# Performance work log

Hardware: AMD Instinct MI355X
Metric: run time of the kernel (lower is better)

## Reference

```python
import jax, jax.numpy as jnp
import numpy as np

B, S, M, D, H, NH = 8, 1024, 2048, 512, 512, 8  # batch, seq, mem slots, memory_dim, hidden_dim, heads
THRESHOLD = 0.5
DECAY = 0.95


def setup_inputs() -> dict:
    key = jax.random.key(0)
    ks = jax.random.split(key, 16)
    def w(k, shape, s=0.02):
        return jax.random.normal(k, shape, jnp.float32) * s
    z = lambda n: jnp.zeros((n,), jnp.float32)
    return {
        'new_info': jax.random.normal(ks[0], (B, S, D), jnp.float32),
        'memory_bank': jax.random.normal(ks[1], (B, M, D), jnp.float32),
        'W_in': w(ks[2], (D, H)), 'b_in': z(H),
        'Wq': w(ks[3], (H, H)), 'bq': z(H),
        'Wk': w(ks[4], (H, H)), 'bk': z(H),
        'Wv': w(ks[5], (H, H)), 'bv': z(H),
        'Wo': w(ks[6], (H, H)), 'bo': z(H),
        'Wi1': w(ks[7], (H, H // 2)), 'bi1': z(H // 2),
        'Wi2': w(ks[8], (H // 2, 1)), 'bi2': z(1),
        'Wu1': w(ks[9], (2 * H, H)), 'bu1': z(H),
        'Wu2': w(ks[10], (H, H)), 'bu2': z(H),
    }


def _mha(q, k, v, Wq, bq, Wk, bk, Wv, bv, Wo, bo):
    # torch nn.MultiheadAttention math (batch_first, eval mode / no dropout)
    b, mq, h = q.shape
    d = h // NH
    qh = (q @ Wq + bq).reshape(b, mq, NH, d)
    kh = (k @ Wk + bk).reshape(b, -1, NH, d)
    vh = (v @ Wv + bv).reshape(b, -1, NH, d)
    scores = jnp.einsum('bqhd,bkhd->bhqk', qh, kh) / np.float32(np.sqrt(d))
    attn = jax.nn.softmax(scores, axis=-1)
    out = jnp.einsum('bhqk,bkhd->bqhd', attn, vh).reshape(b, mq, h)
    return out @ Wo + bo


def reference(new_info, memory_bank, W_in, b_in, Wq, bq, Wk, bk, Wv, bv, Wo, bo,
              Wi1, bi1, Wi2, bi2, Wu1, bu1, Wu2, bu2):
    # project new info + memory into hidden space
    info_proj = new_info @ W_in + b_in                       # [B,S,H]
    mem_proj = memory_bank @ W_in + b_in                     # [B,M,H]
    # per-token importance (sigmoid MLP)
    imp = jax.nn.sigmoid(jax.nn.relu(info_proj @ Wi1 + bi1) @ Wi2 + bi2)[..., 0]  # [B,S]
    # cross-attention: memory slots attend to new tokens -> per-slot write weights
    attn_out = _mha(mem_proj, info_proj, info_proj, Wq, bq, Wk, bk, Wv, bv, Wo, bo)  # [B,M,H]
    # scale write weights by importance (vectorized reading of the original broadcast)
    write_weights = attn_out * jnp.mean(imp, axis=1)[:, None, None]  # [B,M,H]
    # write-position selection: argmax over memory slots (importance scalar is positive,
    # so in the original all qualifying tokens of a batch pick the same slot)
    pos = jnp.argmax(jnp.mean(write_weights, axis=-1), axis=1)      # [B]
    mask = imp > THRESHOLD                                          # [B,S]
    exists = jnp.any(mask, axis=1)                                  # [B]
    # original loop overwrites the slot for each qualifying s, always reading the
    # ORIGINAL memory_bank -> final value comes from the LAST qualifying token
    s_star = S - 1 - jnp.argmax(mask[:, ::-1], axis=1)              # [B]
    bidx = jnp.arange(B)
    sel = new_info[bidx, s_star]                                    # [B,D]
    old = memory_bank[bidx, pos]                                    # [B,D]
    comb = jnp.concatenate([old, sel], axis=-1)                     # [B,2D]
    upd = jnp.tanh(jax.nn.relu(comb @ Wu1 + bu1) @ Wu2 + bu2)       # [B,H]
    ww = write_weights[bidx, pos]                                   # [B,H]
    new_mem = jnp.where(exists[:, None], old + upd * ww, old)
    updated = memory_bank.at[bidx, pos].set(new_mem)
    # forgetting: memory_age defaults to zeros -> decay_rate**0 == 1 (kept for fidelity)
    decay = jnp.power(jnp.float32(DECAY), jnp.zeros((M,), jnp.float32))
    updated = updated * decay[None, :, None]
    return updated, write_weights, imp
```

## Files before the change

kernel.cpp:

```cpp
#include <hip/hip_runtime.h>
#include <hip/hip_bf16.h>
#include <math.h>

#define BB 8
#define SS 1024
#define MM 2048
#define DD 512
#define HH 512
#define NHEAD 8
#define DHEAD 64

typedef __attribute__((ext_vector_type(8))) short short8;
typedef __attribute__((ext_vector_type(4))) float f32x4;
typedef unsigned short us;

__device__ __forceinline__ us bf_hi(float x) {
    __hip_bfloat16 h = __float2bfloat16(x);
    return *reinterpret_cast<const us*>(&h);
}
__device__ __forceinline__ float bf_f(us h) {
    return __uint_as_float(((unsigned)h) << 16);
}
__device__ __forceinline__ void split_pack4(float a, float b, float c, float d,
                                            uint2& hp, uint2& lp) {
    us h0 = bf_hi(a), h1 = bf_hi(b), h2 = bf_hi(c), h3 = bf_hi(d);
    hp.x = (unsigned)h0 | ((unsigned)h1 << 16);
    hp.y = (unsigned)h2 | ((unsigned)h3 << 16);
    us l0 = bf_hi(a - bf_f(h0)), l1 = bf_hi(b - bf_f(h1));
    us l2 = bf_hi(c - bf_f(h2)), l3 = bf_hi(d - bf_f(h3));
    lp.x = (unsigned)l0 | ((unsigned)l1 << 16);
    lp.y = (unsigned)l2 | ((unsigned)l3 << 16);
}
__device__ __forceinline__ uint2 pack4_hi(float a, float b, float c, float d) {
    uint2 hp;
    hp.x = (unsigned)bf_hi(a) | ((unsigned)bf_hi(b) << 16);
    hp.y = (unsigned)bf_hi(c) | ((unsigned)bf_hi(d) << 16);
    return hp;
}

__device__ __forceinline__ void gload_lds16(const void* g, void* l) {
    __builtin_amdgcn_global_load_lds(
        (__attribute__((address_space(1))) void*)(g),
        (__attribute__((address_space(3))) void*)(l), 16, 0, 0);
}

struct TSB {
    const float* src[6];
    us* dh[6];
    us* dl[6];
    int nc[6];
};

__global__ __launch_bounds__(256) void prep_all(
    const float* __restrict__ x, float* __restrict__ cpy,
    us* __restrict__ hi, us* __restrict__ lo, int n8, float* __restrict__ zbuf,
    const float* __restrict__ bk, const float* __restrict__ bv,
    float* __restrict__ bkv,
    const float* __restrict__ b_in, const float* __restrict__ Wq,
    const float* __restrict__ bq, float* __restrict__ bq_eff, TSB a)
{
    __shared__ float tile[32][33];
    const int blk = blockIdx.x, tid = threadIdx.x;
    if (blk >= 2066) {
        const int t = blk - 2066;
        const int wsel = t >> 8;
        const int n0 = (t & 15) * 32, k0 = ((t >> 4) & 15) * 32;
        const int ncols = a.nc[wsel];
        if (n0 >= ncols) return;
        const float* W = a.src[wsel];
        {
            const int r = tid >> 3, c = (tid & 7) * 4;
            const float4 v = *(const float4*)(W + (size_t)(k0 + r) * ncols + n0 + c);
            tile[r][c + 0] = v.x; tile[r][c + 1] = v.y;
            tile[r][c + 2] = v.z; tile[r][c + 3] = v.w;
        }
        __syncthreads();
        {
            const int n = tid >> 3, k = (tid & 7) * 4;
            uint2 hp, lp;
            split_pack4(tile[k + 0][n], tile[k + 1][n], tile[k + 2][n], tile[k + 3][n], hp, lp);
            *(uint2*)(a.dh[wsel] + (size_t)(n0 + n) * 512 + k0 + k) = hp;
            *(uint2*)(a.dl[wsel] + (size_t)(n0 + n) * 512 + k0 + k) = lp;
        }
        return;
    }
    if (blk >= 2064) {
        const int n = (blk - 2064) * 256 + tid;
        float v = bq[n];
        for (int k = 0; k < 512; ++k) v = fmaf(b_in[k], Wq[(size_t)k * 512 + n], v);
        bq_eff[n] = v;
        return;
    }
    if (blk >= 2060) {
        const int i = (blk - 2060) * 256 + tid;
        bkv[i] = (i < 512) ? bk[i] : bv[i - 512];
        return;
    }
    if (blk >= 2048) {
        const int i = (blk - 2048) * 2048 + tid * 8;
        *(float4*)(zbuf + i) = make_float4(0.f, 0.f, 0.f, 0.f);
        *(float4*)(zbuf + i + 4) = make_float4(0.f, 0.f, 0.f, 0.f);
        return;
    }
    const int stride = 2048 * 256;
    for (int i = blk * 256 + tid; i < n8; i += stride) {
        const float4 va = *(const float4*)(x + (size_t)i * 8);
        const float4 vb = *(const float4*)(x + (size_t)i * 8 + 4);
        *(float4*)(cpy + (size_t)i * 8) = va;
        *(float4*)(cpy + (size_t)i * 8 + 4) = vb;
        uint2 h0, l0, h1, l1;
        split_pack4(va.x, va.y, va.z, va.w, h0, l0);
        split_pack4(vb.x, vb.y, vb.z, vb.w, h1, l1);
        *(uint2*)(hi + (size_t)i * 8) = h0;
        *(uint2*)(hi + (size_t)i * 8 + 4) = h1;
        *(uint2*)(lo + (size_t)i * 8) = l0;
        *(uint2*)(lo + (size_t)i * 8 + 4) = l1;
    }
}

#define GEMM_F32A_BODY(K_)                                                          \
    f32x4 acc[4][4];                                                                \
    _Pragma("unroll")                                                               \
    for (int i = 0; i < 4; ++i)                                                     \
        _Pragma("unroll")                                                           \
        for (int j = 0; j < 4; ++j)                                                 \
            _Pragma("unroll")                                                       \
            for (int r = 0; r < 4; ++r) acc[i][j][r] = 0.f;                         \
    const int ar = tid >> 4;                                                        \
    const int ak = (tid & 15) * 4;                                                  \
    int bsrow[4], bsf[4], bsoff[4];                                                 \
    _Pragma("unroll")                                                               \
    for (int it = 0; it < 4; ++it) {                                                \
        const int s = tid + 256 * it;                                               \
        bsrow[it] = s >> 3;                                                         \
        bsf[it] = s & 7;                                                            \
        bsoff[it] = bsrow[it] * 64 + ((bsf[it] ^ (bsrow[it] & 7)) << 3);            \
    }                                                                               \
    for (int k0 = 0; k0 < (K_); k0 += 64) {                                         \
        __syncthreads();                                                            \
        _Pragma("unroll")                                                           \
        for (int p = 0; p < 8; ++p) {                                               \
            const int r = p * 16 + ar;                                              \
            const float4 av = *(const float4*)(A + (size_t)(m0 + r) * (K_) + k0 + ak); \
            const int aoff = r * 128 + (((ak >> 3) ^ (r & 7)) << 4) + ((tid & 1) << 3); \
            uint2 hp, lp;                                                           \
            split_pack4(av.x, av.y, av.z, av.w, hp, lp);                            \
            *(uint2*)((char*)sAh + aoff) = hp;                                      \
            *(uint2*)((char*)sAl + aoff) = lp;                                      \
        }                                                                           \
        _Pragma("unroll")                                                           \
        for (int it = 0; it < 4; ++it) {                                            \
            const size_t bo = (size_t)(n0 + bsrow[it]) * (K_) + k0 + bsf[it] * 8;   \
            *(uint4*)(sBh + bsoff[it]) = *(const uint4*)(Bh + bo);                  \
            *(uint4*)(sBl + bsoff[it]) = *(const uint4*)(Bl + bo);                  \
        }                                                                           \
        __syncthreads();                                                            \
        _Pragma("unroll")                                                           \
        for (int ks = 0; ks < 2; ++ks) {                                            \
            short8 afh[4], afl[4], bfh[4], bfl[4];                                  \
            _Pragma("unroll")                                                       \
            for (int i = 0; i < 4; ++i) {                                           \
                const int row = wm * 64 + i * 16 + fr;                              \
                const int off = row * 128 + (((ks * 4 + fq4) ^ (row & 7)) << 4);    \
                afh[i] = *(const short8*)((const char*)sAh + off);                  \
                afl[i] = *(const short8*)((const char*)sAl + off);                  \
            }                                                                       \
            _Pragma("unroll")                                                       \
            for (int j = 0; j < 4; ++j) {                                           \
                const int row = wn * 64 + j * 16 + fr;                              \
                const int off = row * 128 + (((ks * 4 + fq4) ^ (row & 7)) << 4);    \
                bfh[j] = *(const short8*)((const char*)sBh + off);                  \
                bfl[j] = *(const short8*)((const char*)sBl + off);                  \
            }                                                                       \
            _Pragma("unroll")                                                       \
            for (int i = 0; i < 4; ++i)                                             \
                _Pragma("unroll")                                                   \
                for (int j = 0; j < 4; ++j) {                                       \
                    acc[i][j] = __builtin_amdgcn_mfma_f32_16x16x32_bf16(afh[i], bfh[j], acc[i][j], 0, 0, 0); \
                    acc[i][j] = __builtin_amdgcn_mfma_f32_16x16x32_bf16(afh[i], bfl[j], acc[i][j], 0, 0, 0); \
                    acc[i][j] = __builtin_amdgcn_mfma_f32_16x16x32_bf16(afl[i], bfh[j], acc[i][j], 0, 0, 0); \
                }                                                                   \
        }                                                                           \
    }

__global__ __launch_bounds__(256) void gemm_info_winq(
    const float* __restrict__ new_info,
    const us* __restrict__ wtin_h, const us* __restrict__ wtin_l,
    const float* __restrict__ b_in,
    us* __restrict__ Oh, us* __restrict__ Ol,
    const float* __restrict__ W_in,
    const us* __restrict__ wtq_h, const us* __restrict__ wtq_l,
    us* __restrict__ wtinq_h, us* __restrict__ wtinq_l)
{
    __shared__ us sm[32768];
    us* sAh = sm;            us* sAl = sm + 8192;
    us* sBh = sm + 16384;    us* sBl = sm + 24576;
    const int tid = threadIdx.x, lane = tid & 63;
    const int wid = tid >> 6, wm = wid >> 1, wn = wid & 1;
    const int fr = lane & 15, fq4 = lane >> 4;
    const int id = blockIdx.x;
    const bool isInfo = (id < 256);
    int m0, n0;
    const float* A;
    const us *Bh, *Bl;
    if (isInfo) {
        m0 = (id >> 2) * 128; n0 = (id & 3) * 128;
        A = new_info; Bh = wtin_h; Bl = wtin_l;
    } else {
        const int t = id - 256;
        m0 = (t >> 2) * 128; n0 = (t & 3) * 128;
        A = W_in; Bh = wtq_h; Bl = wtq_l;
    }
    GEMM_F32A_BODY(512)

    if (isInfo) {
#pragma unroll
        for (int j = 0; j < 4; ++j) {
            const int col = n0 + wn * 64 + j * 16 + fr;
            const float bj = b_in[col];
#pragma unroll
            for (int i = 0; i < 4; ++i)
#pragma unroll
                for (int r = 0; r < 4; ++r) {
                    const int row = m0 + wm * 64 + i * 16 + fq4 * 4 + r;
                    const float v = acc[i][j][r] + bj;
                    const us hv = bf_hi(v);
                    Oh[(size_t)row * 512 + col] = hv;
                    Ol[(size_t)row * 512 + col] = bf_hi(v - bf_f(hv));
                }
        }
    } else {
#pragma unroll
        for (int j = 0; j < 4; ++j) {
            const int col = n0 + wn * 64 + j * 16 + fr;
#pragma unroll
            for (int i = 0; i < 4; ++i)
#pragma unroll
                for (int r = 0; r < 4; ++r) {
                    const int row = m0 + wm * 64 + i * 16 + fq4 * 4 + r;
                    const float v = acc[i][j][r];
                    const us hv = bf_hi(v);
                    wtinq_h[(size_t)col * 512 + row] = hv;
                    wtinq_l[(size_t)col * 512 + row] = bf_hi(v - bf_f(hv));
                }
        }
    }
}

#define GEMM_PS_CORE(AhP, AlP, BhP, BlP, rsA_, K_)                                  \
    us* sAh = sm;            us* sAl = sm + 8192;                                   \
    us* sBh = sm + 16384;    us* sBl = sm + 24576;                                  \
    f32x4 acc[4][4];                                                                \
    _Pragma("unroll")                                                               \
    for (int i = 0; i < 4; ++i)                                                     \
        _Pragma("unroll")                                                           \
        for (int j = 0; j < 4; ++j)                                                 \
            _Pragma("unroll")                                                       \
            for (int r = 0; r < 4; ++r) acc[i][j][r] = 0.f;                         \
    const int fp = lane & 7, rsub = lane >> 3;                                      \
    const us* gsrc = (wid == 0) ? (AhP) : (wid == 1) ? (AlP)                        \
                   : (wid == 2) ? (BhP) : (BlP);                                    \
    const int grow0 = (wid < 2) ? m0 : n0;                                          \
    const int grs = (wid < 2) ? (rsA_) : (K_);                                      \
    us* lbase = sm + wid * 8192;                                                    \
    for (int k0 = 0; k0 < (K_); k0 += 64) {                                         \
        __syncthreads();                                                            \
        _Pragma("unroll")                                                           \
        for (int i = 0; i < 16; ++i) {                                              \
            const int row = i * 8 + rsub;                                           \
            const us* g = gsrc + (size_t)(grow0 + row) * grs + k0 +                 \
                          ((fp ^ (row & 7)) << 3);                                  \
            gload_lds16(g, lbase + i * 512);                                        \
        }                                                                           \
        __syncthreads();                                                            \
        _Pragma("unroll")                                                           \
        for (int ks = 0; ks < 2; ++ks) {                                            \
            short8 afh[4], afl[4], bfh[4], bfl[4];                                  \
            _Pragma("unroll")                                                       \
            for (int i = 0; i < 4; ++i) {                                           \
                const int row = wm * 64 + i * 16 + fr;                              \
                const int off = row * 128 + (((ks * 4 + fq4) ^ (row & 7)) << 4);    \
                afh[i] = *(const short8*)((const char*)sAh + off);                  \
                afl[i] = *(const short8*)((const char*)sAl + off);                  \
            }                                                                       \
            _Pragma("unroll")                                                       \
            for (int j = 0; j < 4; ++j) {                                           \
                const int row = wn * 64 + j * 16 + fr;                              \
                const int off = row * 128 + (((ks * 4 + fq4) ^ (row & 7)) << 4);    \
                bfh[j] = *(const short8*)((const char*)sBh + off);                  \
                bfl[j] = *(const short8*)((const char*)sBl + off);                  \
            }                                                                       \
            _Pragma("unroll")                                                       \
            for (int i = 0; i < 4; ++i)                                             \
                _Pragma("unroll")                                                   \
                for (int j = 0; j < 4; ++j) {                                       \
                    acc[i][j] = __builtin_amdgcn_mfma_f32_16x16x32_bf16(afh[i], bfh[j], acc[i][j], 0, 0, 0); \
                    acc[i][j] = __builtin_amdgcn_mfma_f32_16x16x32_bf16(afh[i], bfl[j], acc[i][j], 0, 0, 0); \
                    acc[i][j] = __builtin_amdgcn_mfma_f32_16x16x32_bf16(afl[i], bfh[j], acc[i][j], 0, 0, 0); \
                }                                                                   \
        }                                                                           \
    }

__global__ __launch_bounds__(256) void gemm_qkvh1_ps(
    const us* __restrict__ mbh, const us* __restrict__ mbl,
    const us* __restrict__ wtinq_h, const us* __restrict__ wtinq_l,
    const float* __restrict__ bq_eff,
    us* __restrict__ qsph, us* __restrict__ qspl,
    const us* __restrict__ iph, const us* __restrict__ ipl,
    const us* __restrict__ wtkv_h, const us* __restrict__ wtkv_l,
    const float* __restrict__ bkv,
    us* __restrict__ Kh, us* __restrict__ Kl,
    us* __restrict__ Vth, us* __restrict__ Vtl,
    const us* __restrict__ wti1_h, const us* __restrict__ wti1_l,
    const float* __restrict__ bi1, const float* __restrict__ Wi2,
    float* __restrict__ logit)
{
    __shared__ us sm[32768];
    const int tid = threadIdx.x, lane = tid & 63;
    const int wid = tid >> 6, wm = wid >> 1, wn = wid & 1;
    const int fr = lane & 15, fq4 = lane >> 4;
    const int id = blockIdx.x;
    int m0, n0;
    const us *Ah, *Al, *Bh, *Bl;
    if (id < 512) {
        m0 = (id >> 2) * 128; n0 = (id & 3) * 128;
        Ah = mbh; Al = mbl; Bh = wtinq_h; Bl = wtinq_l;
    } else if (id < 1024) {
        const int t = id - 512;
        m0 = (t >> 3) * 128; n0 = (t & 7) * 128;
        Ah = iph; Al = ipl; Bh = wtkv_h; Bl = wtkv_l;
    } else {
        const int t = id - 1024;
        m0 = (t >> 1) * 128; n0 = (t & 1) * 128;
        Ah = iph; Al = ipl; Bh = wti1_h; Bl = wti1_l;
    }
    GEMM_PS_CORE(Ah, Al, Bh, Bl, 512, 512)

    if (id < 512) {
#pragma unroll
        for (int j = 0; j < 4; ++j) {
            const int col = n0 + wn * 64 + j * 16 + fr;
            const float bj = bq_eff[col];
#pragma unroll
            for (int i = 0; i < 4; ++i)
#pragma unroll
                for (int r = 0; r < 4; ++r) {
                    const int row = m0 + wm * 64 + i * 16 + fq4 * 4 + r;
                    const float v = acc[i][j][r] + bj;
                    const us hv = bf_hi(v);
                    qsph[(size_t)row * 512 + col] = hv;
                    qspl[(size_t)row * 512 + col] = bf_hi(v - bf_f(hv));
                }
        }
    } else if (id < 1024 && n0 < 512) {
#pragma unroll
        for (int j = 0; j < 4; ++j) {
            const int col = n0 + wn * 64 + j * 16 + fr;
            const float bj = bkv[col];
#pragma unroll
            for (int i = 0; i < 4; ++i)
#pragma unroll
                for (int r = 0; r < 4; ++r) {
                    const int row = m0 + wm * 64 + i * 16 + fq4 * 4 + r;
                    const float v = (acc[i][j][r] + bj) * 0.125f;
                    const us hv = bf_hi(v);
                    Kh[(size_t)row * 512 + col] = hv;
                    Kl[(size_t)row * 512 + col] = bf_hi(v - bf_f(hv));
                }
        }
    } else if (id < 1024) {
#pragma unroll
        for (int j = 0; j < 4; ++j) {
            const int col = n0 + wn * 64 + j * 16 + fr;
            const float bj = bkv[col];
            const int d = col - 512;
#pragma unroll
            for (int i = 0; i < 4; ++i) {
                const int row0 = m0 + wm * 64 + i * 16 + fq4 * 4;
                uint2 hp, lp;
                split_pack4(acc[i][j][0] + bj, acc[i][j][1] + bj,
                            acc[i][j][2] + bj, acc[i][j][3] + bj, hp, lp);
                const size_t vo = ((size_t)(row0 >> 10) * 512 + d) * 1024 + (row0 & 1023);
                *(uint2*)(Vth + vo) = hp;
                *(uint2*)(Vtl + vo) = lp;
            }
        }
    } else {
        float wsum[4][4];
#pragma unroll
        for (int i = 0; i < 4; ++i)
#pragma unroll
            for (int r = 0; r < 4; ++r) wsum[i][r] = 0.f;
#pragma unroll
        for (int j = 0; j < 4; ++j) {
            const int col = n0 + wn * 64 + j * 16 + fr;
            const float bj = bi1[col];
            const float w2 = Wi2[col];
#pragma unroll
            for (int i = 0; i < 4; ++i)
#pragma unroll
                for (int r = 0; r < 4; ++r) {
                    const float v = fmaxf(acc[i][j][r] + bj, 0.f);
                    wsum[i][r] = fmaf(v, w2, wsum[i][r]);
                }
        }
        __syncthreads();
        float* red = (float*)sm;
        if (tid < 128) red[tid] = 0.f;
        __syncthreads();
#pragma unroll
        for (int i = 0; i < 4; ++i)
#pragma unroll
            for (int r = 0; r < 4; ++r)
                atomicAdd(&red[wm * 64 + i * 16 + fq4 * 4 + r], wsum[i][r]);
        __syncthreads();
        if (tid < 128) atomicAdd(&logit[m0 + tid], red[tid]);
    }
}

__global__ __launch_bounds__(256) void gemm_wo_ps(
    const us* __restrict__ Ah, const us* __restrict__ Al,
    const us* __restrict__ Bh, const us* __restrict__ Bl,
    const float* __restrict__ bias, float* __restrict__ C,
    const float* __restrict__ rowscale, float* __restrict__ rowmeanv)
{
    __shared__ us sm[32768];
    const int tid = threadIdx.x, lane = tid & 63;
    const int wid = tid >> 6, wm = wid >> 1, wn = wid & 1;
    const int fr = lane & 15, fq4 = lane >> 4;
    const int m0 = blockIdx.y * 128, n0 = blockIdx.x * 128;
    GEMM_PS_CORE(Ah, Al, Bh, Bl, 512, 512)

    float rsum[4][4];
#pragma unroll
    for (int i = 0; i < 4; ++i)
#pragma unroll
        for (int r = 0; r < 4; ++r) rsum[i][r] = 0.f;

#pragma unroll
    for (int j = 0; j < 4; ++j) {
        const int col = n0 + wn * 64 + j * 16 + fr;
        const float bj = bias[col];
#pragma unroll
        for (int i = 0; i < 4; ++i)
#pragma unroll
            for (int r = 0; r < 4; ++r) {
                const int row = m0 + wm * 64 + i * 16 + fq4 * 4 + r;
                const float v = (acc[i][j][r] + bj) * rowscale[row / MM];
                C[(size_t)row * 512 + col] = v;
                rsum[i][r] += v;
            }
    }

    __syncthreads();
    float* red = (float*)sm;
    if (tid < 128) red[tid] = 0.f;
    __syncthreads();
#pragma unroll
    for (int i = 0; i < 4; ++i)
#pragma unroll
        for (int r = 0; r < 4; ++r)
            atomicAdd(&red[wm * 64 + i * 16 + fq4 * 4 + r], rsum[i][r]);
    __syncthreads();
    if (tid < 128) atomicAdd(&rowmeanv[m0 + tid], red[tid] * (1.0f / 512.0f));
}

__global__ __launch_bounds__(256) void attn_mfma(
    const us* __restrict__ Qh, const us* __restrict__ Ql,
    const us* __restrict__ Kh, const us* __restrict__ Kl,
    const us* __restrict__ Vth, const us* __restrict__ Vtl,
    us* __restrict__ aoh, us* __restrict__ aol,
    const float* __restrict__ logit, const float* __restrict__ bi2,
    float* __restrict__ imp, float* __restrict__ imp_mean,
    int* __restrict__ s_star, int* __restrict__ exists)
{
    __shared__ us sm[20480];
    const int tid = threadIdx.x, lane = tid & 63, w = tid >> 6;

    if (blockIdx.x >= 2048) {
        const int b = blockIdx.x - 2048;
        const float b0 = bi2[0];
        float sum = 0.f; int last = -1;
        for (int s = tid; s < SS; s += 256) {
            const float ip = 1.0f / (1.0f + expf(-(logit[b * SS + s] + b0)));
            imp[b * SS + s] = ip;
            sum += ip;
            if (ip > 0.5f) last = s;
        }
#pragma unroll
        for (int m = 1; m < 64; m <<= 1) {
            sum += __shfl_xor(sum, m);
            last = max(last, __shfl_xor(last, m));
        }
        float* ssum = (float*)sm;
        int* slast = (int*)(sm + 16);
        if (lane == 0) { ssum[w] = sum; slast[w] = last; }
        __syncthreads();
        if (tid == 0) {
            const float t = ssum[0] + ssum[1] + ssum[2] + ssum[3];
            const int ml = max(max(slast[0], slast[1]), max(slast[2], slast[3]));
            imp_mean[b] = t / (float)SS;
            exists[b] = (ml >= 0) ? 1 : 0;
            s_star[b] = (ml >= 0) ? ml : (SS - 1);
        }
        return;
    }

    us* sKh = sm;            us* sKl = sm + 4096;
    us* sVh = sm + 8192;     us* sVl = sm + 12288;
    us* sPh = sm + 16384;

    const int fr = lane & 15, fq4 = lane >> 4;

    const int wg = blockIdx.x;
    const int xcd = wg & 7, ix = wg >> 3;
    const int mt = ix & 31;
    const int pair = xcd + 8 * (ix >> 5);
    const int h = pair & 7, b = pair >> 3;
    const int m0 = mt * 64;

    const us* Qgh = Qh + ((size_t)(b * MM + m0)) * 512 + h * DHEAD;
    const us* Qgl = Ql + ((size_t)(b * MM + m0)) * 512 + h * DHEAD;
    const us* Kgh = Kh + ((size_t)b * SS) * 512 + h * DHEAD;
    const us* Kgl = Kl + ((size_t)b * SS) * 512 + h * DHEAD;
    const us* Vgh = Vth + ((size_t)b * 512 + h * DHEAD) * 1024;
    const us* Vgl = Vtl + ((size_t)b * 512 + h * DHEAD) * 1024;
    us* Oh = aoh + ((size_t)(b * MM + m0)) * 512 + h * DHEAD;
    us* Ol = aol + ((size_t)(b * MM + m0)) * 512 + h * DHEAD;

    short8 qfh[2], qfl[2];
#pragma unroll
    for (int ks = 0; ks < 2; ++ks) {
        const size_t qo = (size_t)(w * 16 + fr) * 512 + ks * 32 + fq4 * 8;
        qfh[ks] = *(const short8*)(Qgh + qo);
        qfl[ks] = *(const short8*)(Qgl + qo);
    }

    const int fp = lane & 7;
    const int rsub = lane >> 3;
    const bool isK = (w < 2);
    const us* gA = (w == 0) ? Kgh : (w == 1) ? Kgl : (w == 2) ? Vgh : Vgl;
    us* lbase = sm + w * 4096;

    f32x4 oacc[4];
#pragma unroll
    for (int j = 0; j < 4; ++j)
#pragma unroll
        for (int r = 0; r < 4; ++r) oacc[j][r] = 0.f;
    float mrun = -1e30f, lrun = 0.f;

    for (int t = 0; t < SS / 64; ++t) {
        __syncthreads();
        if (isK) {
#pragma unroll
            for (int i = 0; i < 8; ++i) {
                const int row = i * 8 + rsub;
                const us* g = gA + (size_t)(t * 64 + row) * 512 + ((fp ^ (row & 7)) << 3);
                gload_lds16(g, lbase + i * 512);
            }
        } else {
#pragma unroll
            for (int i = 0; i < 8; ++i) {
                const int row = i * 8 + rsub;
                const us* g = gA + (size_t)row * 1024 + t * 64 + ((fp ^ (row & 7)) << 3);
                gload_lds16(g, lbase + i * 512);
            }
        }
        __syncthreads();

        f32x4 stt[4];
#pragma unroll
        for (int fs = 0; fs < 4; ++fs)
#pragma unroll
            for (int r = 0; r < 4; ++r) stt[fs][r] = 0.f;
        __builtin_amdgcn_s_setprio(1);
#pragma unroll
        for (int ks = 0; ks < 2; ++ks) {
            short8 kfh[4], kfl[4];
#pragma unroll
            for (int fs = 0; fs < 4; ++fs) {
                const int row = fs * 16 + fr;
                const int off = row * 128 + (((ks * 4 + fq4) ^ (row & 7)) << 4);
                kfh[fs] = *(const short8*)((const char*)sKh + off);
                kfl[fs] = *(const short8*)((const char*)sKl + off);
            }
#pragma unroll
            for (int fs = 0; fs < 4; ++fs) {
                stt[fs] = __builtin_amdgcn_mfma_f32_16x16x32_bf16(kfh[fs], qfh[ks], stt[fs], 0, 0, 0);
                stt[fs] = __builtin_amdgcn_mfma_f32_16x16x32_bf16(kfh[fs], qfl[ks], stt[fs], 0, 0, 0);
                stt[fs] = __builtin_amdgcn_mfma_f32_16x16x32_bf16(kfl[fs], qfh[ks], stt[fs], 0, 0, 0);
            }
        }
        __builtin_amdgcn_s_setprio(0);

        float mx = stt[0][0];
#pragma unroll
        for (int fs = 0; fs < 4; ++fs)
#pragma unroll
            for (int r = 0; r < 4; ++r) mx = fmaxf(mx, stt[fs][r]);
        mx = fmaxf(mx, __shfl_xor(mx, 16));
        mx = fmaxf(mx, __shfl_xor(mx, 32));
        const bool grow = __any(mx > mrun);
        float scf = 1.f;
        if (grow) {
            const float nm = fmaxf(mrun, mx);
            scf = __expf(mrun - nm);
            mrun = nm;
        }
        float ps = 0.f;
#pragma unroll
        for (int fs = 0; fs < 4; ++fs)
#pragma unroll
            for (int r = 0; r < 4; ++r) {
                const float p = __expf(stt[fs][r] - mrun);
                stt[fs][r] = p;
                ps += p;
            }
        ps += __shfl_xor(ps, 16);
        ps += __shfl_xor(ps, 32);
        lrun = lrun * scf + ps;

#pragma unroll
        for (int fs = 0; fs < 4; ++fs) {
            const int q = w * 16 + fr;
            const int flog = (fs << 1) | (fq4 >> 1);
            const int off = q * 128 + ((flog ^ (q & 7)) << 4) + ((fq4 & 1) << 3);
            *(uint2*)((char*)sPh + off) = pack4_hi(stt[fs][0], stt[fs][1],
                                                  stt[fs][2], stt[fs][3]);
        }

        if (grow) {
#pragma unroll
            for (int r = 0; r < 4; ++r) {
                const float scv = __shfl(scf, fq4 * 4 + r);
#pragma unroll
                for (int fd = 0; fd < 4; ++fd) oacc[fd][r] *= scv;
            }
        }

        __builtin_amdgcn_s_setprio(1);
#pragma unroll
        for (int ks = 0; ks < 2; ++ks) {
            short8 pfh, vfh[4], vfl[4];
            {
                const int row = w * 16 + fr;
                const int off = row * 128 + (((ks * 4 + fq4) ^ (row & 7)) << 4);
                pfh = *(const short8*)((const char*)sPh + off);
            }
#pragma unroll
            for (int fd = 0; fd < 4; ++fd) {
                const int row = fd * 16 + fr;
                const int off = row * 128 + (((ks * 4 + fq4) ^ (row & 7)) << 4);
                vfh[fd] = *(const short8*)((const char*)sVh + off);
                vfl[fd] = *(const short8*)((const char*)sVl + off);
            }
#pragma unroll
            for (int fd = 0; fd < 4; ++fd) {
                oacc[fd] = __builtin_amdgcn_mfma_f32_16x16x32_bf16(pfh, vfh[fd], oacc[fd], 0, 0, 0);
                oacc[fd] = __builtin_amdgcn_mfma_f32_16x16x32_bf16(pfh, vfl[fd], oacc[fd], 0, 0, 0);
            }
        }
        __builtin_amdgcn_s_setprio(0);
    }

#pragma unroll
    for (int r = 0; r < 4; ++r) {
        const float inv = 1.0f / __shfl(lrun, fq4 * 4 + r);
        const int q = w * 16 + fq4 * 4 + r;
#pragma unroll
        for (int fd = 0; fd < 4; ++fd) {
            const float v = oacc[fd][r] * inv;
            const us hv = bf_hi(v);
            Oh[(size_t)q * 512 + fd * 16 + fr] = hv;
            Ol[(size_t)q * 512 + fd * 16 + fr] = bf_hi(v - bf_f(hv));
        }
    }
}

__global__ __launch_bounds__(256) void argmax_update(
    const float* __restrict__ rm,
    const float* __restrict__ mb, const float* __restrict__ ni,
    const float* __restrict__ Wu1, const float* __restrict__ bu1,
    const float* __restrict__ Wu2, const float* __restrict__ bu2,
    const float* __restrict__ wwp, const int* __restrict__ s_star,
    const int* __restrict__ exists, float* __restrict__ outu)
{
    const int b = blockIdx.x, tid = threadIdx.x;
    __shared__ float comb[2 * DD];
    __shared__ float hu[HH];
    __shared__ float sv[4]; __shared__ int si[4];
    __shared__ int spos;

    {
        float best = -3.0e38f; int bidx = 1 << 30;
        for (int m = tid; m < MM; m += 256) {
            const float v = rm[b * MM + m];
            if (v > best || (v == best && m < bidx)) { best = v; bidx = m; }
        }
#pragma unroll
        for (int msk = 1; msk < 64; msk <<= 1) {
            const float ov = __shfl_xor(best, msk);
            const int oi = __shfl_xor(bidx, msk);
            if (ov > best || (ov == best && oi < bidx)) { best = ov; bidx = oi; }
        }
        if ((tid & 63) == 0) { sv[tid >> 6] = best; si[tid >> 6] = bidx; }
        __syncthreads();
        if (tid == 0) {
            for (int w = 1; w < 4; ++w)
                if (sv[w] > best || (sv[w] == best && si[w] < bidx)) { best = sv[w]; bidx = si[w]; }
            spos = bidx;
        }
        __syncthreads();
    }

    const int p = spos, ss = s_star[b], ex = exists[b];
    const float* oldp = mb + ((size_t)(b * MM + p)) * DD;
    const float* selp = ni + ((size_t)(b * SS + ss)) * DD;
    for (int i = tid; i < DD; i += 256) { comb[i] = oldp[i]; comb[DD + i] = selp[i]; }
    __syncthreads();
#pragma unroll
    for (int t = 0; t < 2; ++t) {
        const int n = tid + t * 256;
        float a0 = 0.f, a1 = 0.f, a2 = 0.f, a3 = 0.f;
        for (int k = 0; k < 2 * DD; k += 4) {
            a0 = fmaf(comb[k + 0], Wu1[(size_t)(k + 0) * HH + n], a0);
            a1 = fmaf(comb[k + 1], Wu1[(size_t)(k + 1) * HH + n], a1);
            a2 = fmaf(comb[k + 2], Wu1[(size_t)(k + 2) * HH + n], a2);
            a3 = fmaf(comb[k + 3], Wu1[(size_t)(k + 3) * HH + n], a3);
        }
        hu[n] = fmaxf(bu1[n] + ((a0 + a1) + (a2 + a3)), 0.f);
    }
    __syncthreads();
#pragma unroll
    for (int t = 0; t < 2; ++t) {
        const int n = tid + t * 256;
        float a0 = 0.f, a1 = 0.f, a2 = 0.f, a3 = 0.f;
        for (int k = 0; k < HH; k += 4) {
            a0 = fmaf(hu[k + 0], Wu2[(size_t)(k + 0) * HH + n], a0);
            a1 = fmaf(hu[k + 1], Wu2[(size_t)(k + 1) * HH + n], a1);
            a2 = fmaf(hu[k + 2], Wu2[(size_t)(k + 2) * HH + n], a2);
            a3 = fmaf(hu[k + 3], Wu2[(size_t)(k + 3) * HH + n], a3);
        }
        const float upd = tanhf(bu2[n] + ((a0 + a1) + (a2 + a3)));
        const float wwv = wwp[((size_t)(b * MM + p)) * HH + n];
        const float ov = oldp[n];
        outu[((size_t)(b * MM + p)) * DD + n] = ex ? fmaf(upd, wwv, ov) : ov;
    }
}

extern "C" void kernel_launch(void* const* d_in, const int* in_sizes, int n_in,
                              void* d_out, int out_size, void* d_ws, size_t ws_size,
                              hipStream_t stream)
{
    const float* new_info    = (const float*)d_in[0];
    const float* memory_bank = (const float*)d_in[1];
    const float* W_in = (const float*)d_in[2];  const float* b_in = (const float*)d_in[3];
    const float* Wq   = (const float*)d_in[4];  const float* bq   = (const float*)d_in[5];
    const float* Wk   = (const float*)d_in[6];  const float* bk   = (const float*)d_in[7];
    const float* Wv   = (const float*)d_in[8];  const float* bv   = (const float*)d_in[9];
    const float* Wo   = (const float*)d_in[10]; const float* bo   = (const float*)d_in[11];
    const float* Wi1  = (const float*)d_in[12]; const float* bi1  = (const float*)d_in[13];
    const float* Wi2  = (const float*)d_in[14]; const float* bi2  = (const float*)d_in[15];
    const float* Wu1  = (const float*)d_in[16]; const float* bu1  = (const float*)d_in[17];
    const float* Wu2  = (const float*)d_in[18]; const float* bu2  = (const float*)d_in[19];

    float* out = (float*)d_out;
    float* out_updated = out;
    float* out_ww      = out + (size_t)BB * MM * HH;
    float* out_imp     = out + 2 * (size_t)BB * MM * HH;

    float* ws = (float*)d_ws;
    float* qsp_rg    = ws;
    float* ip_sp     = qsp_rg + 8388608;
    float* mb_sp     = ip_sp + 4194304;
    float* kvreg     = mb_sp + 8388608;
    float* wtf       = kvreg + 8388608;
    float* bq_eff    = wtf + 1703936;
    float* bkv       = bq_eff + 512;
    float* rowmeanv  = bkv + 1024;
    float* logit     = rowmeanv + 16384;
    float* imp_mean  = logit + 8192;
    int*   istar     = (int*)(imp_mean + BB);
    int*   iexists   = istar + BB;

    us* qsph = (us*)qsp_rg;
    us* qspl = qsph + 8388608;
    us* iph = (us*)ip_sp;
    us* ipl = iph + 4194304;
    us* mbh = (us*)mb_sp;
    us* mbl = mbh + 8388608;
    us* Kh  = (us*)kvreg;
    us* Kl  = Kh + 4194304;
    us* Vth = Kl + 4194304;
    us* Vtl = Vth + 4194304;

    us* wtin_h  = (us*)wtf;            us* wtin_l  = wtin_h + 262144;
    us* wtq_h   = wtin_l + 262144;     us* wtq_l   = wtq_h + 262144;
    us* wtkv_h  = wtq_l + 262144;      us* wtkv_l  = wtkv_h + 524288;
    us* wto_h   = wtkv_l + 524288;     us* wto_l   = wto_h + 262144;
    us* wtinq_h = wto_l + 262144;      us* wtinq_l = wtinq_h + 262144;
    us* wti1_h  = wtinq_l + 262144;    us* wti1_l  = wti1_h + 131072;

    const dim3 blk(256);

    TSB ts;
    ts.src[0] = W_in; ts.dh[0] = wtin_h;          ts.dl[0] = wtin_l;          ts.nc[0] = 512;
    ts.src[1] = Wq;   ts.dh[1] = wtq_h;           ts.dl[1] = wtq_l;           ts.nc[1] = 512;
    ts.src[2] = Wk;   ts.dh[2] = wtkv_h;          ts.dl[2] = wtkv_l;          ts.nc[2] = 512;
    ts.src[3] = Wv;   ts.dh[3] = wtkv_h + 262144; ts.dl[3] = wtkv_l + 262144; ts.nc[3] = 512;
    ts.src[4] = Wo;   ts.dh[4] = wto_h;           ts.dl[4] = wto_l;           ts.nc[4] = 512;
    ts.src[5] = Wi1;  ts.dh[5] = wti1_h;          ts.dl[5] = wti1_l;          ts.nc[5] = 256;
    prep_all<<<dim3(2066 + 1536), blk, 0, stream>>>(memory_bank, out_updated,
                                                    mbh, mbl, 1048576, rowmeanv,
                                                    bk, bv, bkv, b_in, Wq, bq,
                                                    bq_eff, ts);

    gemm_info_winq<<<dim3(272), blk, 0, stream>>>(new_info, wtin_h, wtin_l, b_in,
                                                  iph, ipl, W_in, wtq_h, wtq_l,
                                                  wtinq_h, wtinq_l);

    gemm_qkvh1_ps<<<dim3(1152), blk, 0, stream>>>(mbh, mbl, wtinq_h, wtinq_l,
                                                  bq_eff, qsph, qspl,
                                                  iph, ipl, wtkv_h, wtkv_l, bkv,
                                                  Kh, Kl, Vth, Vtl,
                                                  wti1_h, wti1_l, bi1, Wi2, logit);

    attn_mfma<<<dim3(2056), blk, 0, stream>>>(qsph, qspl, Kh, Kl, Vth, Vtl,
                                              mbh, mbl, logit, bi2, out_imp,
                                              imp_mean, istar, iexists);

    gemm_wo_ps<<<dim3(4, 128), blk, 0, stream>>>(mbh, mbl, wto_h, wto_l,
                                                 bo, out_ww, imp_mean, rowmeanv);

    argmax_update<<<dim3(BB), blk, 0, stream>>>(rowmeanv, memory_bank, new_info,
                                                Wu1, bu1, Wu2, bu2, out_ww,
                                                istar, iexists, out_updated);
}
```

Measured before the change: 409.1 us.

## Fold W_in into K/V/importance weights and use exp2 softmax

Precomputes W_in@Wk, W_in@Wv and W_in@Wi1 (and the matching effective biases), so K, V and the importance hidden layer are computed straight from new_info. This drops the separate info_proj GEMM, its split bf16 hi/lo intermediate buffer and the extra pass over it. The K scaling now includes log2(e), so the softmax can use native exp2 instead of expf. The cost is a small extra weight-fusion kernel and a slightly different rounding path for the combined weights.

```diff
diff --git a/kernel.cpp b/kernel.cpp
--- a/kernel.cpp
+++ b/kernel.cpp
@@ -13,6 +13,8 @@
 typedef __attribute__((ext_vector_type(8))) short short8;
 typedef __attribute__((ext_vector_type(4))) float f32x4;
 typedef unsigned short us;
+
+#define KLOG2E 0.18033688011112042f
 
 __device__ __forceinline__ us bf_hi(float x) {
     __hip_bfloat16 h = __float2bfloat16(x);
@@ -55,14 +57,17 @@
     const float* __restrict__ x, float* __restrict__ cpy,
     us* __restrict__ hi, us* __restrict__ lo, int n8, float* __restrict__ zbuf,
     const float* __restrict__ bk, const float* __restrict__ bv,
-    float* __restrict__ bkv,
+    const float* __restrict__ Wk, const float* __restrict__ Wv,
+    float* __restrict__ bkv_eff,
     const float* __restrict__ b_in, const float* __restrict__ Wq,
-    const float* __restrict__ bq, float* __restrict__ bq_eff, TSB a)
+    const float* __restrict__ bq, float* __restrict__ bq_eff,
+    const float* __restrict__ Wi1, const float* __restrict__ bi1,
+    float* __restrict__ bi1_eff, TSB a)
 {
     __shared__ float tile[32][33];
     const int blk = blockIdx.x, tid = threadIdx.x;
-    if (blk >= 2066) {
-        const int t = blk - 2066;
+    if (blk >= 2067) {
+        const int t = blk - 2067;
         const int wsel = t >> 8;
         const int n0 = (t & 15) * 32, k0 = ((t >> 4) & 15) * 32;
         const int ncols = a.nc[wsel];
@@ -84,6 +89,13 @@
         }
         return;
     }
+    if (blk >= 2066) {
+        const int n = tid;
+        float v = bi1[n];
+        for (int k = 0; k < 512; ++k) v = fmaf(b_in[k], Wi1[(size_t)k * 256 + n], v);
+        bi1_eff[n] = v;
+        return;
+    }
     if (blk >= 2064) {
         const int n = (blk - 2064) * 256 + tid;
         float v = bq[n];
@@ -93,7 +105,16 @@
     }
     if (blk >= 2060) {
         const int i = (blk - 2060) * 256 + tid;
-        bkv[i] = (i < 512) ? bk[i] : bv[i - 512];
+        if (i < 512) {
+            float v = bk[i];
+            for (int k = 0; k < 512; ++k) v = fmaf(b_in[k], Wk[(size_t)k * 512 + i], v);
+            bkv_eff[i] = v;
+        } else {
+            const int n = i - 512;
+            float v = bv[n];
+            for (int k = 0; k < 512; ++k) v = fmaf(b_in[k], Wv[(size_t)k * 512 + n], v);
+            bkv_eff[i] = v;
+        }
         return;
     }
     if (blk >= 2048) {
@@ -183,70 +204,6 @@
         }                                                                           \
     }
 
-__global__ __launch_bounds__(256) void gemm_info_winq(
-    const float* __restrict__ new_info,
-    const us* __restrict__ wtin_h, const us* __restrict__ wtin_l,
-    const float* __restrict__ b_in,
-    us* __restrict__ Oh, us* __restrict__ Ol,
-    const float* __restrict__ W_in,
-    const us* __restrict__ wtq_h, const us* __restrict__ wtq_l,
-    us* __restrict__ wtinq_h, us* __restrict__ wtinq_l)
-{
-    __shared__ us sm[32768];
-    us* sAh = sm;            us* sAl = sm + 8192;
-    us* sBh = sm + 16384;    us* sBl = sm + 24576;
-    const int tid = threadIdx.x, lane = tid & 63;
-    const int wid = tid >> 6, wm = wid >> 1, wn = wid & 1;
-    const int fr = lane & 15, fq4 = lane >> 4;
-    const int id = blockIdx.x;
-    const bool isInfo = (id < 256);
-    int m0, n0;
-    const float* A;
-    const us *Bh, *Bl;
-    if (isInfo) {
-        m0 = (id >> 2) * 128; n0 = (id & 3) * 128;
-        A = new_info; Bh = wtin_h; Bl = wtin_l;
-    } else {
-        const int t = id - 256;
-        m0 = (t >> 2) * 128; n0 = (t & 3) * 128;
-        A = W_in; Bh = wtq_h; Bl = wtq_l;
-    }
-    GEMM_F32A_BODY(512)
-
-    if (isInfo) {
-#pragma unroll
-        for (int j = 0; j < 4; ++j) {
-            const int col = n0 + wn * 64 + j * 16 + fr;
-            const float bj = b_in[col];
-#pragma unroll
-            for (int i = 0; i < 4; ++i)
-#pragma unroll
-                for (int r = 0; r < 4; ++r) {
-                    const int row = m0 + wm * 64 + i * 16 + fq4 * 4 + r;
-                    const float v = acc[i][j][r] + bj;
-                    const us hv = bf_hi(v);
-                    Oh[(size_t)row * 512 + col] = hv;
-                    Ol[(size_t)row * 512 + col] = bf_hi(v - bf_f(hv));
-                }
-        }
-    } else {
-#pragma unroll
-        for (int j = 0; j < 4; ++j) {
-            const int col = n0 + wn * 64 + j * 16 + fr;
-#pragma unroll
-            for (int i = 0; i < 4; ++i)
-#pragma unroll
-                for (int r = 0; r < 4; ++r) {
-                    const int row = m0 + wm * 64 + i * 16 + fq4 * 4 + r;
-                    const float v = acc[i][j][r];
-                    const us hv = bf_hi(v);
-                    wtinq_h[(size_t)col * 512 + row] = hv;
-                    wtinq_l[(size_t)col * 512 + row] = bf_hi(v - bf_f(hv));
-                }
-        }
-    }
-}
-
 #define GEMM_PS_CORE(AhP, AlP, BhP, BlP, rsA_, K_)                                  \
     us* sAh = sm;            us* sAl = sm + 8192;                                   \
     us* sBh = sm + 16384;    us* sBl = sm + 24576;                                  \
@@ -301,18 +258,73 @@
         }                                                                           \
     }
 
-__global__ __launch_bounds__(256) void gemm_qkvh1_ps(
+__global__ __launch_bounds__(256) void gemm_wfuse(
+    const float* __restrict__ W_in,
+    const us* __restrict__ wtq_h, const us* __restrict__ wtq_l,
+    const us* __restrict__ wtk_h, const us* __restrict__ wtk_l,
+    const us* __restrict__ wtv_h, const us* __restrict__ wtv_l,
+    const us* __restrict__ wti1_h, const us* __restrict__ wti1_l,
+    us* __restrict__ wtinq_h, us* __restrict__ wtinq_l,
+    us* __restrict__ wtinkv_h, us* __restrict__ wtinkv_l,
+    us* __restrict__ wtini1_h, us* __restrict__ wtini1_l)
+{
+    __shared__ us sm[32768];
+    us* sAh = sm;            us* sAl = sm + 8192;
+    us* sBh = sm + 16384;    us* sBl = sm + 24576;
+    const int tid = threadIdx.x, lane = tid & 63;
+    const int wid = tid >> 6, wm = wid >> 1, wn = wid & 1;
+    const int fr = lane & 15, fq4 = lane >> 4;
+    const int id = blockIdx.x;
+    int m0, n0, coff = 0;
+    const us *Bh, *Bl;
+    us *Oh, *Ol;
+    if (id < 16) {
+        m0 = (id >> 2) * 128; n0 = (id & 3) * 128;
+        Bh = wtq_h; Bl = wtq_l; Oh = wtinq_h; Ol = wtinq_l;
+    } else if (id < 32) {
+        const int t = id - 16;
+        m0 = (t >> 2) * 128; n0 = (t & 3) * 128;
+        Bh = wtk_h; Bl = wtk_l; Oh = wtinkv_h; Ol = wtinkv_l;
+    } else if (id < 48) {
+        const int t = id - 32;
+        m0 = (t >> 2) * 128; n0 = (t & 3) * 128;
+        Bh = wtv_h; Bl = wtv_l; Oh = wtinkv_h; Ol = wtinkv_l; coff = 512;
+    } else {
+        const int t = id - 48;
+        m0 = (t >> 1) * 128; n0 = (t & 1) * 128;
+        Bh = wti1_h; Bl = wti1_l; Oh = wtini1_h; Ol = wtini1_l;
+    }
+    const float* A = W_in;
+    GEMM_F32A_BODY(512)
+
+#pragma unroll
+    for (int j = 0; j < 4; ++j) {
+        const int col = n0 + wn * 64 + j * 16 + fr + coff;
+#pragma unroll
+        for (int i = 0; i < 4; ++i)
+#pragma unroll
+            for (int r = 0; r < 4; ++r) {
+                const int row = m0 + wm * 64 + i * 16 + fq4 * 4 + r;
+                const float v = acc[i][j][r];
+                const us hv = bf_hi(v);
+                Oh[(size_t)col * 512 + row] = hv;
+                Ol[(size_t)col * 512 + row] = bf_hi(v - bf_f(hv));
+            }
+    }
+}
+
+__global__ __launch_bounds__(256) void gemm_qkvh1(
     const us* __restrict__ mbh, const us* __restrict__ mbl,
     const us* __restrict__ wtinq_h, const us* __restrict__ wtinq_l,
     const float* __restrict__ bq_eff,
     us* __restrict__ qsph, us* __restrict__ qspl,
-    const us* __restrict__ iph, const us* __restrict__ ipl,
-    const us* __restrict__ wtkv_h, const us* __restrict__ wtkv_l,
-    const float* __restrict__ bkv,
+    const float* __restrict__ new_info,
+    const us* __restrict__ wtinkv_h, const us* __restrict__ wtinkv_l,
+    const float* __restrict__ bkv_eff,
     us* __restrict__ Kh, us* __restrict__ Kl,
     us* __restrict__ Vth, us* __restrict__ Vtl,
-    const us* __restrict__ wti1_h, const us* __restrict__ wti1_l,
-    const float* __restrict__ bi1, const float* __restrict__ Wi2,
+    const us* __restrict__ wtini1_h, const us* __restrict__ wtini1_l,
+    const float* __restrict__ bi1_eff, const float* __restrict__ Wi2,
     float* __restrict__ logit)
 {
     __shared__ us sm[32768];
@@ -320,23 +332,10 @@
     const int wid = tid >> 6, wm = wid >> 1, wn = wid & 1;
     const int fr = lane & 15, fq4 = lane >> 4;
     const int id = blockIdx.x;
-    int m0, n0;
-    const us *Ah, *Al, *Bh, *Bl;
+
     if (id < 512) {
-        m0 = (id >> 2) * 128; n0 = (id & 3) * 128;
-        Ah = mbh; Al = mbl; Bh = wtinq_h; Bl = wtinq_l;
-    } else if (id < 1024) {
-        const int t = id - 512;
-        m0 = (t >> 3) * 128; n0 = (t & 7) * 128;
-        Ah = iph; Al = ipl; Bh = wtkv_h; Bl = wtkv_l;
-    } else {
-        const int t = id - 1024;
-        m0 = (t >> 1) * 128; n0 = (t & 1) * 128;
-        Ah = iph; Al = ipl; Bh = wti1_h; Bl = wti1_l;
-    }
-    GEMM_PS_CORE(Ah, Al, Bh, Bl, 512, 512)
-
-    if (id < 512) {
+        const int m0 = (id >> 2) * 128, n0 = (id & 3) * 128;
+        GEMM_PS_CORE(mbh, mbl, wtinq_h, wtinq_l, 512, 512)
 #pragma unroll
         for (int j = 0; j < 4; ++j) {
             const int col = n0 + wn * 64 + j * 16 + fr;
@@ -352,49 +351,69 @@
                     qspl[(size_t)row * 512 + col] = bf_hi(v - bf_f(hv));
                 }
         }
-    } else if (id < 1024 && n0 < 512) {
+        return;
+    }
+
+    us* sAh = sm;            us* sAl = sm + 8192;
+    us* sBh = sm + 16384;    us* sBl = sm + 24576;
+    if (id < 1024) {
+        const int t = id - 512;
+        const int m0 = (t >> 3) * 128, n0 = (t & 7) * 128;
+        const float* A = new_info;
+        const us* Bh = wtinkv_h; const us* Bl = wtinkv_l;
+        GEMM_F32A_BODY(512)
+        if (n0 < 512) {
+#pragma unroll
+            for (int j = 0; j < 4; ++j) {
+                const int col = n0 + wn * 64 + j * 16 + fr;
+                const float bj = bkv_eff[col];
+#pragma unroll
+                for (int i = 0; i < 4; ++i)
+#pragma unroll
+                    for (int r = 0; r < 4; ++r) {
+                        const int row = m0 + wm * 64 + i * 16 + fq4 * 4 + r;
+                        const float v = (acc[i][j][r] + bj) * KLOG2E;
+                        const us hv = bf_hi(v);
+                        Kh[(size_t)row * 512 + col] = hv;
+                        Kl[(size_t)row * 512 + col] = bf_hi(v - bf_f(hv));
+                    }
+            }
+        } else {
+#pragma unroll
+            for (int j = 0; j < 4; ++j) {
+                const int col = n0 + wn * 64 + j * 16 + fr;
+                const float bj = bkv_eff[col];
+                const int d = col - 512;
+#pragma unroll
+                for (int i = 0; i < 4; ++i) {
+                    const int row0 = m0 + wm * 64 + i * 16 + fq4 * 4;
+                    uint2 hp, lp;
+                    split_pack4(acc[i][j][0] + bj, acc[i][j][1] + bj,
+                                acc[i][j][2] + bj, acc[i][j][3] + bj, hp, lp);
+                    const size_t vo = ((size_t)(row0 >> 10) * 512 + d) * 1024 + (row0 & 1023);
+                    *(uint2*)(Vth + vo) = hp;
+                    *(uint2*)(Vtl + vo) = lp;
+                }
+            }
+        }
+        return;
+    }
+
+    {
+        const int t = id - 1024;
+        const int m0 = (t >> 1) * 128, n0 = (t & 1) * 128;
+        const float* A = new_info;
+        const us* Bh = wtini1_h; const us* Bl = wtini1_l;
+        GEMM_F32A_BODY(512)
+        float wsum[4][4];
+#pragma unroll
+        for (int i = 0; i < 4; ++i)
+#pragma unroll
+            for (int r = 0; r < 4; ++r) wsum[i][r] = 0.f;
 #pragma unroll
         for (int j = 0; j < 4; ++j) {
             const int col = n0 + wn * 64 + j * 16 + fr;
-            const float bj = bkv[col];
-#pragma unroll
-            for (int i = 0; i < 4; ++i)
-#pragma unroll
-                for (int r = 0; r < 4; ++r) {
-                    const int row = m0 + wm * 64 + i * 16 + fq4 * 4 + r;
-                    const float v = (acc[i][j][r] + bj) * 0.125f;
-                    const us hv = bf_hi(v);
-                    Kh[(size_t)row * 512 + col] = hv;
-                    Kl[(size_t)row * 512 + col] = bf_hi(v - bf_f(hv));
-                }
-        }
-    } else if (id < 1024) {
-#pragma unroll
-        for (int j = 0; j < 4; ++j) {
-            const int col = n0 + wn * 64 + j * 16 + fr;
-            const float bj = bkv[col];
-            const int d = col - 512;
-#pragma unroll
-            for (int i = 0; i < 4; ++i) {
-                const int row0 = m0 + wm * 64 + i * 16 + fq4 * 4;
-                uint2 hp, lp;
-                split_pack4(acc[i][j][0] + bj, acc[i][j][1] + bj,
-                            acc[i][j][2] + bj, acc[i][j][3] + bj, hp, lp);
-                const size_t vo = ((size_t)(row0 >> 10) * 512 + d) * 1024 + (row0 & 1023);
-                *(uint2*)(Vth + vo) = hp;
-                *(uint2*)(Vtl + vo) = lp;
-            }
-        }
-    } else {
-        float wsum[4][4];
-#pragma unroll
-        for (int i = 0; i < 4; ++i)
-#pragma unroll
-            for (int r = 0; r < 4; ++r) wsum[i][r] = 0.f;
-#pragma unroll
-        for (int j = 0; j < 4; ++j) {
-            const int col = n0 + wn * 64 + j * 16 + fr;
-            const float bj = bi1[col];
+            const float bj = bi1_eff[col];
             const float w2 = Wi2[col];
 #pragma unroll
             for (int i = 0; i < 4; ++i)
@@ -604,7 +623,7 @@
         float scf = 1.f;
         if (grow) {
             const float nm = fmaxf(mrun, mx);
-            scf = __expf(mrun - nm);
+            scf = __builtin_amdgcn_exp2f(mrun - nm);
             mrun = nm;
         }
         float ps = 0.f;
@@ -612,7 +631,7 @@
         for (int fs = 0; fs < 4; ++fs)
 #pragma unroll
             for (int r = 0; r < 4; ++r) {
-                const float p = __expf(stt[fs][r] - mrun);
+                const float p = __builtin_amdgcn_exp2f(stt[fs][r] - mrun);
                 stt[fs][r] = p;
                 ps += p;
             }
@@ -771,13 +790,13 @@
 
     float* ws = (float*)d_ws;
     float* qsp_rg    = ws;
-    float* ip_sp     = qsp_rg + 8388608;
-    float* mb_sp     = ip_sp + 4194304;
+    float* mb_sp     = qsp_rg + 8388608;
     float* kvreg     = mb_sp + 8388608;
     float* wtf       = kvreg + 8388608;
-    float* bq_eff    = wtf + 1703936;
-    float* bkv       = bq_eff + 512;
-    float* rowmeanv  = bkv + 1024;
+    float* bq_eff    = wtf + 2097152;
+    float* bkv_eff   = bq_eff + 512;
+    float* bi1_eff   = bkv_eff + 1024;
+    float* rowmeanv  = bi1_eff + 256;
     float* logit     = rowmeanv + 16384;
     float* imp_mean  = logit + 8192;
     int*   istar     = (int*)(imp_mean + BB);
@@ -785,8 +804,6 @@
 
     us* qsph = (us*)qsp_rg;
     us* qspl = qsph + 8388608;
-    us* iph = (us*)ip_sp;
-    us* ipl = iph + 4194304;
     us* mbh = (us*)mb_sp;
     us* mbl = mbh + 8388608;
     us* Kh  = (us*)kvreg;
@@ -794,36 +811,42 @@
     us* Vth = Kl + 4194304;
     us* Vtl = Vth + 4194304;
 
-    us* wtin_h  = (us*)wtf;            us* wtin_l  = wtin_h + 262144;
-    us* wtq_h   = wtin_l + 262144;     us* wtq_l   = wtq_h + 262144;
-    us* wtkv_h  = wtq_l + 262144;      us* wtkv_l  = wtkv_h + 524288;
-    us* wto_h   = wtkv_l + 524288;     us* wto_l   = wto_h + 262144;
-    us* wtinq_h = wto_l + 262144;      us* wtinq_l = wtinq_h + 262144;
-    us* wti1_h  = wtinq_l + 262144;    us* wti1_l  = wti1_h + 131072;
+    us* wtq_h    = (us*)wtf;            us* wtq_l    = wtq_h + 262144;
+    us* wtk_h    = wtq_l + 262144;      us* wtk_l    = wtk_h + 262144;
+    us* wtv_h    = wtk_l + 262144;      us* wtv_l    = wtv_h + 262144;
+    us* wto_h    = wtv_l + 262144;      us* wto_l    = wto_h + 262144;
+    us* wti1_h   = wto_l + 262144;      us* wti1_l   = wti1_h + 131072;
+    us* wtinq_h  = wti1_l + 131072;     us* wtinq_l  = wtinq_h + 262144;
+    us* wtinkv_h = wtinq_l + 262144;    us* wtinkv_l = wtinkv_h + 524288;
+    us* wtini1_h = wtinkv_l + 524288;   us* wtini1_l = wtini1_h + 131072;
 
     const dim3 blk(256);
 
     TSB ts;
-    ts.src[0] = W_in; ts.dh[0] = wtin_h;          ts.dl[0] = wtin_l;          ts.nc[0] = 512;
-    ts.src[1] = Wq;   ts.dh[1] = wtq_h;           ts.dl[1] = wtq_l;           ts.nc[1] = 512;
-    ts.src[2] = Wk;   ts.dh[2] = wtkv_h;          ts.dl[2] = wtkv_l;          ts.nc[2] = 512;
-    ts.src[3] = Wv;   ts.dh[3] = wtkv_h + 262144; ts.dl[3] = wtkv_l + 262144; ts.nc[3] = 512;
-    ts.src[4] = Wo;   ts.dh[4] = wto_h;           ts.dl[4] = wto_l;           ts.nc[4] = 512;
-    ts.src[5] = Wi1;  ts.dh[5] = wti1_h;          ts.dl[5] = wti1_l;          ts.nc[5] = 256;
-    prep_all<<<dim3(2066 + 1536), blk, 0, stream>>>(memory_bank, out_updated,
+    ts.src[0] = Wq;  ts.dh[0] = wtq_h;  ts.dl[0] = wtq_l;  ts.nc[0] = 512;
+    ts.src[1] = Wk;  ts.dh[1] = wtk_h;  ts.dl[1] = wtk_l;  ts.nc[1] = 512;
+    ts.src[2] = Wv;  ts.dh[2] = wtv_h;  ts.dl[2] = wtv_l;  ts.nc[2] = 512;
+    ts.src[3] = Wo;  ts.dh[3] = wto_h;  ts.dl[3] = wto_l;  ts.nc[3] = 512;
+    ts.src[4] = Wi1; ts.dh[4] = wti1_h; ts.dl[4] = wti1_l; ts.nc[4] = 256;
+    prep_all<<<dim3(2067 + 1280), blk, 0, stream>>>(memory_bank, out_updated,
                                                     mbh, mbl, 1048576, rowmeanv,
-                                                    bk, bv, bkv, b_in, Wq, bq,
-                                                    bq_eff, ts);
-
-    gemm_info_winq<<<dim3(272), blk, 0, stream>>>(new_info, wtin_h, wtin_l, b_in,
-                                                  iph, ipl, W_in, wtq_h, wtq_l,
-                                                  wtinq_h, wtinq_l);
-
-    gemm_qkvh1_ps<<<dim3(1152), blk, 0, stream>>>(mbh, mbl, wtinq_h, wtinq_l,
-                                                  bq_eff, qsph, qspl,
-                                                  iph, ipl, wtkv_h, wtkv_l, bkv,
-                                                  Kh, Kl, Vth, Vtl,
-                                                  wti1_h, wti1_l, bi1, Wi2, logit);
+                                                    bk, bv, Wk, Wv, bkv_eff,
+                                                    b_in, Wq, bq, bq_eff,
+                                                    Wi1, bi1, bi1_eff, ts);
+
+    gemm_wfuse<<<dim3(56), blk, 0, stream>>>(W_in,
+                                             wtq_h, wtq_l, wtk_h, wtk_l,
+                                             wtv_h, wtv_l, wti1_h, wti1_l,
+                                             wtinq_h, wtinq_l,
+                                             wtinkv_h, wtinkv_l,
+                                             wtini1_h, wtini1_l);
+
+    gemm_qkvh1<<<dim3(1152), blk, 0, stream>>>(mbh, mbl, wtinq_h, wtinq_l,
+                                               bq_eff, qsph, qspl,
+                                               new_info, wtinkv_h, wtinkv_l,
+                                               bkv_eff, Kh, Kl, Vth, Vtl,
+                                               wtini1_h, wtini1_l, bi1_eff,
+                                               Wi2, logit);
 
     attn_mfma<<<dim3(2056), blk, 0, stream>>>(qsph, qspl, Kh, Kl, Vth, Vtl,
                                               mbh, mbl, logit, bi2, out_imp,
```

Result: slower. 492.2 us (+20.3%).
